# Performance work log

Measured on AMD Instinct MI355X. Metric: run time of the kernel, lower is better.

## Reference

```python
import jax, jax.numpy as jnp
import numpy as np

B, S, E, H = 2, 2048, 1024, 16
D = E // H

def setup_inputs() -> dict:
    key = jax.random.key(0)
    ks = jax.random.split(key, 5)
    return {
        "hidden_states": jax.random.normal(ks[0], (B, S, E), dtype=jnp.float32),
        "c_attn_w": jax.random.normal(ks[1], (E, 3 * E), dtype=jnp.float32) * 0.02,
        "c_attn_b": jax.random.normal(ks[2], (3 * E,), dtype=jnp.float32) * 0.02,
        "c_proj_w": jax.random.normal(ks[3], (E, E), dtype=jnp.float32) * 0.02,
        "c_proj_b": jax.random.normal(ks[4], (E,), dtype=jnp.float32) * 0.02,
    }

def reference(hidden_states, c_attn_w, c_attn_b, c_proj_w, c_proj_b):
    x = hidden_states                      # [B, S, E]
    b, s, _ = x.shape
    w_q, w_k, w_v = jnp.split(c_attn_w, 3, axis=1)   # each [E, E]
    q_b, k_b, v_b = jnp.split(c_attn_b, 3, axis=0)   # each [E]

    # value projection
    v = x @ w_v + v_b                                        # [B,S,E]
    v = v.reshape(b, s, H, D).transpose(0, 2, 1, 3)          # [B,H,S,D]

    # fused query: ((x Wq + qb) Wk^T + kb)
    q = (x @ w_q + q_b) @ w_k.T + k_b                        # [B,S,E]
    qh = q.reshape(b, s, H, D).transpose(0, 2, 1, 3)         # [B,H,S,D]

    # key side is RAW hidden states split per head
    kh = x.reshape(b, s, H, D).transpose(0, 2, 1, 3)         # [B,H,S,D]

    scale = 1.0 / jnp.float32(D) ** 0.5
    scores = jnp.einsum("bhqd,bhkd->bhqk",
                        qh.astype(jnp.float32),
                        kh.astype(jnp.float32)) * scale       # [B,H,S,S] fp32

    causal = jnp.tril(jnp.ones((s, s), dtype=bool))
    mask_value = jnp.finfo(jnp.float32).min
    scores = jnp.where(causal[None, None], scores, mask_value)

    probs = jax.nn.softmax(scores, axis=-1).astype(v.dtype)  # [B,H,S,S]

    out = jnp.einsum("bhqk,bhkd->bhqd", probs, v)            # [B,H,S,D]
    out = out.transpose(0, 2, 1, 3).reshape(b, s, E)         # [B,S,E]
    out = out @ c_proj_w + c_proj_b
    return out
```

## Files before the change

### kernel.cpp

```cpp
#include <hip/hip_runtime.h>

typedef __attribute__((ext_vector_type(8))) __bf16 bf16x8;
typedef __attribute__((ext_vector_type(4))) __bf16 bf16x4;
typedef __attribute__((ext_vector_type(4))) float f32x4;

typedef __attribute__((address_space(1))) void as1_void;
typedef __attribute__((address_space(3))) void as3_void;

__device__ __forceinline__ void gl_lds16(const void* g, void* l) {
    __builtin_amdgcn_global_load_lds((const as1_void*)g, (as3_void*)l, 16, 0, 0);
}

__device__ __forceinline__ const bf16x8* swz(const __bf16* base, int row, int chunk) {
    return (const bf16x8*)((const char*)base + row * 128 + ((chunk ^ (row & 7)) * 16));
}

#define QSCALE (0.125f * 1.44269504f)

__global__ __launch_bounds__(256) void prep_kernel(
    const float* __restrict__ x, const float* __restrict__ caw,
    const float* __restrict__ cab, const float* __restrict__ cpw,
    __bf16* __restrict__ xb, __bf16* __restrict__ wvt,
    __bf16* __restrict__ wkn, __bf16* __restrict__ wqn,
    __bf16* __restrict__ wpt, float* __restrict__ bqv)
{
    __shared__ float tile[32 * 33];
    int bid = blockIdx.x;
    int tid = threadIdx.x;
    if (bid < 1024) {
        int nt = bid >> 5, kt = bid & 31;
        int tx = tid & 31, ty = tid >> 5;
        int n0 = nt * 32, k0 = kt * 32;
#pragma unroll
        for (int i = 0; i < 4; ++i)
            tile[(ty + i * 8) * 33 + tx] = caw[(long)(k0 + ty + i * 8) * 3072 + 2048 + n0 + tx];
        __syncthreads();
#pragma unroll
        for (int i = 0; i < 4; ++i)
            wvt[(long)(n0 + ty + i * 8) * 1024 + k0 + tx] = (__bf16)tile[tx * 33 + ty + i * 8];
    } else if (bid < 2048) {
        int v = bid - 1024;
        int nt = v >> 5, kt = v & 31;
        int tx = tid & 31, ty = tid >> 5;
        int n0 = nt * 32, k0 = kt * 32;
#pragma unroll
        for (int i = 0; i < 4; ++i)
            tile[(ty + i * 8) * 33 + tx] = cpw[(long)(k0 + ty + i * 8) * 1024 + n0 + tx];
        __syncthreads();
#pragma unroll
        for (int i = 0; i < 4; ++i)
            wpt[(long)(n0 + ty + i * 8) * 1024 + k0 + tx] = (__bf16)tile[tx * 33 + ty + i * 8];
    } else if (bid < 3072) {
        int e = (bid - 2048) * 1024 + tid * 4;
        int n = e >> 10, k = e & 1023;
        float4 f = *(const float4*)(caw + (long)n * 3072 + 1024 + k);
        bf16x4 o = {(__bf16)f.x, (__bf16)f.y, (__bf16)f.z, (__bf16)f.w};
        *(bf16x4*)(wkn + e) = o;
    } else if (bid < 4096) {
        int e = (bid - 3072) * 1024 + tid * 4;
        int n = e >> 10, k = e & 1023;
        float4 f = *(const float4*)(caw + (long)n * 3072 + k);
        bf16x4 o = {(__bf16)f.x, (__bf16)f.y, (__bf16)f.z, (__bf16)f.w};
        *(bf16x4*)(wqn + e) = o;
    } else if (bid < 8192) {
        long e = (long)(bid - 4096) * 1024 + tid * 4;
        float4 f = *(const float4*)(x + e);
        bf16x4 o = {(__bf16)f.x, (__bf16)f.y, (__bf16)f.z, (__bf16)f.w};
        *(bf16x4*)(xb + e) = o;
    } else {
        int k = bid - 8192;
        int wave = tid >> 6, lane = tid & 63;
        float qv[16];
#pragma unroll
        for (int u = 0; u < 4; ++u) {
            float4 q4 = *(const float4*)(cab + u * 256 + lane * 4);
            qv[u * 4 + 0] = q4.x; qv[u * 4 + 1] = q4.y;
            qv[u * 4 + 2] = q4.z; qv[u * 4 + 3] = q4.w;
        }
        for (int i = 0; i < 16; ++i) {
            int n = k * 64 + wave * 16 + i;
            float s = 0.f;
#pragma unroll
            for (int u = 0; u < 4; ++u) {
                float4 w4 = *(const float4*)(caw + (long)n * 3072 + 1024 + u * 256 + lane * 4);
                s += w4.x * qv[u * 4 + 0] + w4.y * qv[u * 4 + 1]
                   + w4.z * qv[u * 4 + 2] + w4.w * qv[u * 4 + 3];
            }
#pragma unroll
            for (int off = 1; off < 64; off <<= 1) s += __shfl_xor(s, off);
            if (lane == 0) bqv[n] = (s + cab[1024 + n]) * QSCALE;
        }
        if (tid < 64) bqv[1024 + k * 64 + tid] = cab[2048 + k * 64 + tid];
    }
}

template <bool BF16OUT, int BN>
__global__ __launch_bounds__(256) void gemm_bt(
    const __bf16* __restrict__ A, int lda,
    const __bf16* __restrict__ B, int ldb,
    const float* __restrict__ bias,
    void* __restrict__ C, int ldc, int K, float oscale)
{
    constexpr int NT = BN / 32;
    __shared__ __bf16 As[128 * 64];
    __shared__ __bf16 Bs[BN * 64];
    const int tid = threadIdx.x;
    const int lane = tid & 63;
    const int wave = tid >> 6;
    const int quad = lane >> 4, l16 = lane & 15;
    const long m0 = (long)blockIdx.y * 128;
    const long n0 = (long)blockIdx.x * BN;
    const int wm = (wave >> 1) * 64, wn = (wave & 1) * (BN / 2);

    f32x4 acc[4][NT] = {};

    for (int k0 = 0; k0 < K; k0 += 64) {
#pragma unroll
        for (int c = tid; c < (128 + BN) * 8; c += 256) {
            int row = c >> 3, cc = (c & 7) ^ (row & 7);
            if (row < 128)
                gl_lds16(A + (m0 + row) * lda + k0 + cc * 8, As + c * 8);
            else
                gl_lds16(B + (n0 + row - 128) * ldb + k0 + cc * 8, Bs + (c - 1024) * 8);
        }
        __syncthreads();
#pragma unroll
        for (int kk = 0; kk < 2; ++kk) {
            bf16x8 af[4], bfr[NT];
#pragma unroll
            for (int i = 0; i < 4; ++i)
                af[i] = *swz(As, wm + i * 16 + l16, kk * 4 + quad);
#pragma unroll
            for (int j = 0; j < NT; ++j)
                bfr[j] = *swz(Bs, wn + j * 16 + l16, kk * 4 + quad);
#pragma unroll
            for (int i = 0; i < 4; ++i)
#pragma unroll
                for (int j = 0; j < NT; ++j)
                    acc[i][j] = __builtin_amdgcn_mfma_f32_16x16x32_bf16(af[i], bfr[j], acc[i][j], 0, 0, 0);
        }
        __syncthreads();
    }
#pragma unroll
    for (int i = 0; i < 4; ++i) {
        long row = m0 + wm + i * 16 + quad * 4;
#pragma unroll
        for (int j = 0; j < NT; ++j) {
            int col = (int)n0 + wn + j * 16 + l16;
            float bb = bias ? bias[col] : 0.f;
#pragma unroll
            for (int r = 0; r < 4; ++r) {
                float v = (acc[i][j][r] + bb) * oscale;
                if (BF16OUT)
                    ((__bf16*)C)[(row + r) * ldc + col] = (__bf16)v;
                else
                    ((float*)C)[(row + r) * ldc + col] = v;
            }
        }
    }
}

__global__ __launch_bounds__(256) void gemm_qv(
    const __bf16* __restrict__ A,
    const __bf16* __restrict__ B,
    const float* __restrict__ bias,
    __bf16* __restrict__ Qout,
    __bf16* __restrict__ VTout)
{
    __shared__ __bf16 smem[128 * 136];
    __bf16* As = smem;
    __bf16* Bs = smem + 8192;
    const int tid = threadIdx.x;
    const int lane = tid & 63;
    const int wave = tid >> 6;
    const int quad = lane >> 4, l16 = lane & 15;
    const long m0 = (long)blockIdx.y * 128;
    const long n0 = (long)blockIdx.x * 128;
    const int wm = (wave >> 1) * 64, wn = (wave & 1) * 64;

    f32x4 acc[4][4] = {};

    for (int k0 = 0; k0 < 1024; k0 += 64) {
#pragma unroll
        for (int c = tid; c < 2048; c += 256) {
            int row = c >> 3, cc = (c & 7) ^ (row & 7);
            if (row < 128)
                gl_lds16(A + (m0 + row) * 1024 + k0 + cc * 8, As + c * 8);
            else
                gl_lds16(B + (n0 + row - 128) * 1024 + k0 + cc * 8, Bs + (c - 1024) * 8);
        }
        __syncthreads();
#pragma unroll
        for (int kk = 0; kk < 2; ++kk) {
            bf16x8 af[4], bfr[4];
#pragma unroll
            for (int i = 0; i < 4; ++i)
                af[i] = *swz(As, wm + i * 16 + l16, kk * 4 + quad);
#pragma unroll
            for (int j = 0; j < 4; ++j)
                bfr[j] = *swz(Bs, wn + j * 16 + l16, kk * 4 + quad);
#pragma unroll
            for (int i = 0; i < 4; ++i)
#pragma unroll
                for (int j = 0; j < 4; ++j)
                    acc[i][j] = __builtin_amdgcn_mfma_f32_16x16x32_bf16(af[i], bfr[j], acc[i][j], 0, 0, 0);
        }
        __syncthreads();
    }

    if (n0 < 1024) {
#pragma unroll
        for (int i = 0; i < 4; ++i) {
            long row = m0 + wm + i * 16 + quad * 4;
#pragma unroll
            for (int j = 0; j < 4; ++j) {
                int col = (int)n0 + wn + j * 16 + l16;
                float bb = bias[col];
#pragma unroll
                for (int r = 0; r < 4; ++r)
                    Qout[(row + r) * 1024 + col] = (__bf16)(acc[i][j][r] + bb);
            }
        }
    } else {
        __syncthreads();
#pragma unroll
        for (int i = 0; i < 4; ++i) {
#pragma unroll
            for (int j = 0; j < 4; ++j) {
                int col = (int)n0 + wn + j * 16 + l16;
                float bb = bias[col];
                bf16x4 v;
#pragma unroll
                for (int r = 0; r < 4; ++r) v[r] = (__bf16)(acc[i][j][r] + bb);
                *(bf16x4*)(smem + (wn + j * 16 + l16) * 136 + wm + i * 16 + quad * 4) = v;
            }
        }
        __syncthreads();
        const int d0 = (int)n0 - 1024;
        const int bb = (int)(m0 >> 11);
        const int sl = (int)(m0 & 2047);
#pragma unroll
        for (int pass = 0; pass < 16; ++pass) {
            int idx = pass * 256 + tid;
            int n = idx >> 5;
            int mc = (idx & 31) * 4;
            bf16x4 v = *(const bf16x4*)(smem + n * 136 + mc);
            *(bf16x4*)(VTout + ((long)(bb * 1024 + d0 + n)) * 2048 + sl + mc) = v;
        }
    }
}

__global__ __launch_bounds__(512) void attn_kernel(
    const __bf16* __restrict__ Q,
    const __bf16* __restrict__ Xb,
    const __bf16* __restrict__ VT,
    __bf16* __restrict__ O)
{
    __shared__ __bf16 Ks[2 * 8192];
    __shared__ __bf16 Vs[2 * 8192];
    __shared__ __bf16 Ps[8 * 1024];
    const int tid = threadIdx.x;
    const int lane = tid & 63;
    const int wave = tid >> 6;
    const int group = wave >> 2;
    const int w4 = wave & 3;
    const int quad = lane >> 4, l16 = lane & 15;
    const int qa = blockIdx.y;
    const int qb = 31 - qa;
    const int qt = group ? qb : qa;
    const int bh = blockIdx.x;
    const int b = bh >> 4, h = bh & 15;
    const long rowbase = (long)b * 2048;

    const int s0 = tid;
    const int c0 = ((s0 & 7) ^ ((s0 >> 3) & 7)) * 8;

    bf16x8 ones;
#pragma unroll
    for (int i = 0; i < 8; ++i) ones[i] = (__bf16)1.0f;

    bf16x8 qfr[2];
    {
        const __bf16* qp = Q + (rowbase + qt * 64 + w4 * 16 + l16) * 1024 + h * 64 + quad * 8;
        qfr[0] = *(const bf16x8*)(qp);
        qfr[1] = *(const bf16x8*)(qp + 32);
    }

    const __bf16* kp0 = Xb + (rowbase + (s0 >> 3)) * 1024 + h * 64 + c0;
    const __bf16* vp0 = VT + ((long)(b * 1024 + h * 64 + (s0 >> 3))) * 2048 + c0;

    auto stage_tile = [&](int j, int buf, int sub) {
        gl_lds16(kp0 + (long)j * 65536, Ks + buf * 8192 + sub * 4096 + s0 * 8);
        gl_lds16(vp0 + j * 64, Vs + buf * 8192 + sub * 4096 + s0 * 8);
    };
    stage_tile(0, 0, 0);
    stage_tile(1, 0, 1);

    const int nouter = (qb + 2) >> 1;

    f32x4 oacc[4] = {};
    f32x4 lacc = {};
    __bf16* Pw = Ps + wave * 1024;

    for (int jj = 0; jj < nouter; ++jj) {
        __syncthreads();
        if (jj + 1 < nouter) {
            stage_tile(2 * jj + 2, (jj + 1) & 1, 0);
            stage_tile(2 * jj + 3, (jj + 1) & 1, 1);
        }

#pragma unroll
        for (int sub = 0; sub < 2; ++sub) {
            const int j = 2 * jj + sub;
            if (j > qt) continue;
            const __bf16* Kb = Ks + (jj & 1) * 8192 + sub * 4096;
            const __bf16* Vb = Vs + (jj & 1) * 8192 + sub * 4096;

            bf16x8 kf[2][4], vf[2][4];
#pragma unroll
            for (int kk = 0; kk < 2; ++kk)
#pragma unroll
                for (int kt = 0; kt < 4; ++kt) {
                    kf[kk][kt] = *swz(Kb, kt * 16 + l16, kk * 4 + quad);
                    vf[kk][kt] = *swz(Vb, kt * 16 + l16, kk * 4 + quad);
                }

            f32x4 sacc[4] = {};
            __builtin_amdgcn_s_setprio(1);
#pragma unroll
            for (int kk = 0; kk < 2; ++kk)
#pragma unroll
                for (int kt = 0; kt < 4; ++kt)
                    sacc[kt] = __builtin_amdgcn_mfma_f32_16x16x32_bf16(
                        kf[kk][kt], qfr[kk], sacc[kt], 0, 0, 0);
            __builtin_amdgcn_s_setprio(0);

            if (j == qt) {
                const int qloc = w4 * 16 + l16;
#pragma unroll
                for (int kt = 0; kt < 4; ++kt) {
                    bf16x4 pk;
#pragma unroll
                    for (int r = 0; r < 4; ++r) {
                        float s = sacc[kt][r];
                        if (kt * 16 + quad * 4 + r > qloc) s = -1e30f;
                        pk[r] = (__bf16)exp2f(s);
                    }
                    *(bf16x4*)((char*)Pw + l16 * 128 +
                               (((kt * 2 + (quad >> 1)) ^ (l16 & 7)) * 16) + (quad & 1) * 8) = pk;
                }
            } else {
#pragma unroll
                for (int kt = 0; kt < 4; ++kt) {
                    bf16x4 pk;
#pragma unroll
                    for (int r = 0; r < 4; ++r)
                        pk[r] = (__bf16)exp2f(sacc[kt][r]);
                    *(bf16x4*)((char*)Pw + l16 * 128 +
                               (((kt * 2 + (quad >> 1)) ^ (l16 & 7)) * 16) + (quad & 1) * 8) = pk;
                }
            }

            __builtin_amdgcn_s_setprio(1);
#pragma unroll
            for (int kk = 0; kk < 2; ++kk) {
                bf16x8 pf = *swz(Pw, l16, kk * 4 + quad);
                lacc = __builtin_amdgcn_mfma_f32_16x16x32_bf16(ones, pf, lacc, 0, 0, 0);
#pragma unroll
                for (int dt = 0; dt < 4; ++dt)
                    oacc[dt] = __builtin_amdgcn_mfma_f32_16x16x32_bf16(
                        vf[kk][dt], pf, oacc[dt], 0, 0, 0);
            }
            __builtin_amdgcn_s_setprio(0);
        }
    }

    {
        float inv = 1.0f / lacc[0];
        long row = rowbase + qt * 64 + w4 * 16 + l16;
#pragma unroll
        for (int dt = 0; dt < 4; ++dt) {
            bf16x4 ov;
#pragma unroll
            for (int r = 0; r < 4; ++r) ov[r] = (__bf16)(oacc[dt][r] * inv);
            *(bf16x4*)(O + row * 1024 + h * 64 + dt * 16 + quad * 4) = ov;
        }
    }
}

extern "C" void kernel_launch(void* const* d_in, const int* in_sizes, int n_in,
                              void* d_out, int out_size, void* d_ws, size_t ws_size,
                              hipStream_t stream) {
    const float* x   = (const float*)d_in[0];
    const float* caw = (const float*)d_in[1];
    const float* cab = (const float*)d_in[2];
    const float* cpw = (const float*)d_in[3];
    const float* cpb = (const float*)d_in[4];

    char* p = (char*)d_ws;
    auto alloc = [&](size_t bytes) {
        void* r = (void*)p;
        p += (bytes + 255) & ~(size_t)255;
        return r;
    };
    __bf16* xb    = (__bf16*)alloc(4096UL * 1024 * 2);
    __bf16* mtb   = (__bf16*)alloc(1024UL * 1024 * 2);
    __bf16* wvt   = (__bf16*)alloc(1024UL * 1024 * 2);
    __bf16* wkn   = (__bf16*)alloc(1024UL * 1024 * 2);
    __bf16* wqn   = (__bf16*)alloc(1024UL * 1024 * 2);
    __bf16* wpt   = (__bf16*)alloc(1024UL * 1024 * 2);
    float*  bqv   = (float*) alloc(2048UL * 4);
    __bf16* qbuf  = (__bf16*)alloc(4096UL * 1024 * 2);
    __bf16* vt    = (__bf16*)alloc(2048UL * 2048 * 2);
    __bf16* attn  = (__bf16*)alloc(4096UL * 1024 * 2);

    prep_kernel<<<8208, 256, 0, stream>>>(x, caw, cab, cpw, xb, wvt, wkn, wqn, wpt, bqv);

    gemm_bt<true, 32><<<dim3(32, 8), 256, 0, stream>>>(wkn, 1024, wqn, 1024, nullptr,
                                                       (void*)mtb, 1024, 1024, QSCALE);
    gemm_qv<<<dim3(16, 32), 256, 0, stream>>>(xb, mtb, bqv, qbuf, vt);
    attn_kernel<<<dim3(32, 16), 512, 0, stream>>>(qbuf, xb, vt, attn);
    gemm_bt<false, 64><<<dim3(16, 32), 256, 0, stream>>>(attn, 1024, wpt, 1024, cpb,
                                                         d_out, 1024, 1024, 1.0f);
    (void)in_sizes; (void)n_in; (void)out_size; (void)ws_size;
}
```

Baseline: 184.1 us.

## Fuse Wk·Wqᵀ weight GEMM into prep kernel with on-the-fly fp32→bf16 conversion

Removes the separate bf16 conversion of the Wq and Wk slices and the standalone gemm_bt launch that built the fused query matrix. Prep blocks now read fp32 weights directly, convert them to bf16 into LDS, and run the MFMA product inside the prep kernel. This saves one launch and the intermediate bf16 weight round-trip through memory. In exchange the new GEMM blocks use unpipelined synchronous loads, a larger shared-memory footprint for every prep block, and strided fp32 reads.

```diff
diff --git a/kernel.cpp b/kernel.cpp
--- a/kernel.cpp
+++ b/kernel.cpp
@@ -13,6 +13,14 @@
 
 __device__ __forceinline__ const bf16x8* swz(const __bf16* base, int row, int chunk) {
     return (const bf16x8*)((const char*)base + row * 128 + ((chunk ^ (row & 7)) * 16));
+}
+
+__device__ __forceinline__ bf16x8 cvt8(const float* p) {
+    float4 a = *(const float4*)p, b = *(const float4*)(p + 4);
+    bf16x8 o;
+    o[0] = (__bf16)a.x; o[1] = (__bf16)a.y; o[2] = (__bf16)a.z; o[3] = (__bf16)a.w;
+    o[4] = (__bf16)b.x; o[5] = (__bf16)b.y; o[6] = (__bf16)b.z; o[7] = (__bf16)b.w;
+    return o;
 }
 
 #define QSCALE (0.125f * 1.44269504f)
@@ -21,13 +29,14 @@
     const float* __restrict__ x, const float* __restrict__ caw,
     const float* __restrict__ cab, const float* __restrict__ cpw,
     __bf16* __restrict__ xb, __bf16* __restrict__ wvt,
-    __bf16* __restrict__ wkn, __bf16* __restrict__ wqn,
-    __bf16* __restrict__ wpt, float* __restrict__ bqv)
+    __bf16* __restrict__ wpt, float* __restrict__ bqv,
+    __bf16* __restrict__ mtb)
 {
-    __shared__ float tile[32 * 33];
+    __shared__ char smem_u[20480];
     int bid = blockIdx.x;
     int tid = threadIdx.x;
     if (bid < 1024) {
+        float* tile = (float*)smem_u;
         int nt = bid >> 5, kt = bid & 31;
         int tx = tid & 31, ty = tid >> 5;
         int n0 = nt * 32, k0 = kt * 32;
@@ -39,6 +48,7 @@
         for (int i = 0; i < 4; ++i)
             wvt[(long)(n0 + ty + i * 8) * 1024 + k0 + tx] = (__bf16)tile[tx * 33 + ty + i * 8];
     } else if (bid < 2048) {
+        float* tile = (float*)smem_u;
         int v = bid - 1024;
         int nt = v >> 5, kt = v & 31;
         int tx = tid & 31, ty = tid >> 5;
@@ -50,25 +60,13 @@
 #pragma unroll
         for (int i = 0; i < 4; ++i)
             wpt[(long)(n0 + ty + i * 8) * 1024 + k0 + tx] = (__bf16)tile[tx * 33 + ty + i * 8];
-    } else if (bid < 3072) {
-        int e = (bid - 2048) * 1024 + tid * 4;
-        int n = e >> 10, k = e & 1023;
-        float4 f = *(const float4*)(caw + (long)n * 3072 + 1024 + k);
-        bf16x4 o = {(__bf16)f.x, (__bf16)f.y, (__bf16)f.z, (__bf16)f.w};
-        *(bf16x4*)(wkn + e) = o;
-    } else if (bid < 4096) {
-        int e = (bid - 3072) * 1024 + tid * 4;
-        int n = e >> 10, k = e & 1023;
-        float4 f = *(const float4*)(caw + (long)n * 3072 + k);
-        bf16x4 o = {(__bf16)f.x, (__bf16)f.y, (__bf16)f.z, (__bf16)f.w};
-        *(bf16x4*)(wqn + e) = o;
-    } else if (bid < 8192) {
-        long e = (long)(bid - 4096) * 1024 + tid * 4;
+    } else if (bid < 6144) {
+        long e = (long)(bid - 2048) * 1024 + tid * 4;
         float4 f = *(const float4*)(x + e);
         bf16x4 o = {(__bf16)f.x, (__bf16)f.y, (__bf16)f.z, (__bf16)f.w};
         *(bf16x4*)(xb + e) = o;
-    } else {
-        int k = bid - 8192;
+    } else if (bid < 6160) {
+        int k = bid - 6144;
         int wave = tid >> 6, lane = tid & 63;
         float qv[16];
 #pragma unroll
@@ -91,6 +89,61 @@
             if (lane == 0) bqv[n] = (s + cab[1024 + n]) * QSCALE;
         }
         if (tid < 64) bqv[1024 + k * 64 + tid] = cab[2048 + k * 64 + tid];
+    } else {
+        __bf16* As = (__bf16*)smem_u;
+        __bf16* Bs = (__bf16*)(smem_u + 16384);
+        const int v = bid - 6160;
+        const int bx = v & 31, by = v >> 5;
+        const int lane = tid & 63;
+        const int wave = tid >> 6;
+        const int quad = lane >> 4, l16 = lane & 15;
+        const long m0 = (long)by * 128;
+        const long n0 = (long)bx * 32;
+        const int wm = (wave >> 1) * 64, wn = (wave & 1) * 16;
+
+        f32x4 acc[4] = {};
+
+        for (int k0 = 0; k0 < 1024; k0 += 64) {
+            bf16x8 st[5];
+#pragma unroll
+            for (int i = 0; i < 5; ++i) {
+                int c = tid + i * 256;
+                int row = c >> 3, cc = (c & 7) ^ (row & 7);
+                const float* src = (row < 128)
+                    ? caw + (long)(m0 + row) * 3072 + 1024 + k0 + cc * 8
+                    : caw + (long)(n0 + row - 128) * 3072 + k0 + cc * 8;
+                st[i] = cvt8(src);
+            }
+            __syncthreads();
+#pragma unroll
+            for (int i = 0; i < 5; ++i) {
+                int c = tid + i * 256;
+                int row = c >> 3;
+                if (row < 128) *(bf16x8*)(As + c * 8) = st[i];
+                else           *(bf16x8*)(Bs + (c - 1024) * 8) = st[i];
+            }
+            __syncthreads();
+#pragma unroll
+            for (int kk = 0; kk < 2; ++kk) {
+                bf16x8 af[4], bfr;
+#pragma unroll
+                for (int i = 0; i < 4; ++i)
+                    af[i] = *swz(As, wm + i * 16 + l16, kk * 4 + quad);
+                bfr = *swz(Bs, wn + l16, kk * 4 + quad);
+#pragma unroll
+                for (int i = 0; i < 4; ++i)
+                    acc[i] = __builtin_amdgcn_mfma_f32_16x16x32_bf16(af[i], bfr, acc[i], 0, 0, 0);
+            }
+            __syncthreads();
+        }
+#pragma unroll
+        for (int i = 0; i < 4; ++i) {
+            long row = m0 + wm + i * 16 + quad * 4;
+            int col = (int)n0 + wn + l16;
+#pragma unroll
+            for (int r = 0; r < 4; ++r)
+                mtb[(row + r) * 1024 + col] = (__bf16)(acc[i][r] * QSCALE);
+        }
     }
 }
 
@@ -406,18 +459,13 @@
     __bf16* xb    = (__bf16*)alloc(4096UL * 1024 * 2);
     __bf16* mtb   = (__bf16*)alloc(1024UL * 1024 * 2);
     __bf16* wvt   = (__bf16*)alloc(1024UL * 1024 * 2);
-    __bf16* wkn   = (__bf16*)alloc(1024UL * 1024 * 2);
-    __bf16* wqn   = (__bf16*)alloc(1024UL * 1024 * 2);
     __bf16* wpt   = (__bf16*)alloc(1024UL * 1024 * 2);
     float*  bqv   = (float*) alloc(2048UL * 4);
     __bf16* qbuf  = (__bf16*)alloc(4096UL * 1024 * 2);
     __bf16* vt    = (__bf16*)alloc(2048UL * 2048 * 2);
     __bf16* attn  = (__bf16*)alloc(4096UL * 1024 * 2);
 
-    prep_kernel<<<8208, 256, 0, stream>>>(x, caw, cab, cpw, xb, wvt, wkn, wqn, wpt, bqv);
-
-    gemm_bt<true, 32><<<dim3(32, 8), 256, 0, stream>>>(wkn, 1024, wqn, 1024, nullptr,
-                                                       (void*)mtb, 1024, 1024, QSCALE);
+    prep_kernel<<<6416, 256, 0, stream>>>(x, caw, cab, cpw, xb, wvt, wpt, bqv, mtb);
     gemm_qv<<<dim3(16, 32), 256, 0, stream>>>(xb, mtb, bqv, qbuf, vt);
     attn_kernel<<<dim3(32, 16), 512, 0, stream>>>(qbuf, xb, vt, attn);
     gemm_bt<false, 64><<<dim3(16, 32), 256, 0, stream>>>(attn, 1024, wpt, 1024, cpb,
```

Result: slower. 189.1 us (+2.8%).

## Compute query as (xWq+qb)Wk^T+kb instead of precomposing WqWk^T

Applied to the files above, without the earlier changes.

Drops the precomputed fused matrix Wq·Wk^T and the bias GEMV blocks in the prep kernel. It instead runs a full x·Wq+qb GEMM into a temporary buffer, then multiplies that by Wk^T (plus kb and the softmax scale) inside the Q/V GEMM, which now takes a separate A operand per half. This removes the small weight-product GEMM and the per-row bias reduction. In exchange it adds a full-size activation GEMM and an extra round-trip of a 4096x1024 intermediate through memory.

```diff
diff --git a/kernel.cpp b/kernel.cpp
--- a/kernel.cpp
+++ b/kernel.cpp
@@ -19,10 +19,10 @@
 
 __global__ __launch_bounds__(256) void prep_kernel(
     const float* __restrict__ x, const float* __restrict__ caw,
-    const float* __restrict__ cab, const float* __restrict__ cpw,
+    const float* __restrict__ cpw,
     __bf16* __restrict__ xb, __bf16* __restrict__ wvt,
-    __bf16* __restrict__ wkn, __bf16* __restrict__ wqn,
-    __bf16* __restrict__ wpt, float* __restrict__ bqv)
+    __bf16* __restrict__ wpt, __bf16* __restrict__ wqt,
+    __bf16* __restrict__ wkn)
 {
     __shared__ float tile[32 * 33];
     int bid = blockIdx.x;
@@ -51,46 +51,28 @@
         for (int i = 0; i < 4; ++i)
             wpt[(long)(n0 + ty + i * 8) * 1024 + k0 + tx] = (__bf16)tile[tx * 33 + ty + i * 8];
     } else if (bid < 3072) {
-        int e = (bid - 2048) * 1024 + tid * 4;
+        int v = bid - 2048;
+        int nt = v >> 5, kt = v & 31;
+        int tx = tid & 31, ty = tid >> 5;
+        int n0 = nt * 32, k0 = kt * 32;
+#pragma unroll
+        for (int i = 0; i < 4; ++i)
+            tile[(ty + i * 8) * 33 + tx] = caw[(long)(k0 + ty + i * 8) * 3072 + n0 + tx];
+        __syncthreads();
+#pragma unroll
+        for (int i = 0; i < 4; ++i)
+            wqt[(long)(n0 + ty + i * 8) * 1024 + k0 + tx] = (__bf16)tile[tx * 33 + ty + i * 8];
+    } else if (bid < 4096) {
+        int e = (bid - 3072) * 1024 + tid * 4;
         int n = e >> 10, k = e & 1023;
         float4 f = *(const float4*)(caw + (long)n * 3072 + 1024 + k);
         bf16x4 o = {(__bf16)f.x, (__bf16)f.y, (__bf16)f.z, (__bf16)f.w};
         *(bf16x4*)(wkn + e) = o;
-    } else if (bid < 4096) {
-        int e = (bid - 3072) * 1024 + tid * 4;
-        int n = e >> 10, k = e & 1023;
-        float4 f = *(const float4*)(caw + (long)n * 3072 + k);
-        bf16x4 o = {(__bf16)f.x, (__bf16)f.y, (__bf16)f.z, (__bf16)f.w};
-        *(bf16x4*)(wqn + e) = o;
-    } else if (bid < 8192) {
+    } else {
         long e = (long)(bid - 4096) * 1024 + tid * 4;
         float4 f = *(const float4*)(x + e);
         bf16x4 o = {(__bf16)f.x, (__bf16)f.y, (__bf16)f.z, (__bf16)f.w};
         *(bf16x4*)(xb + e) = o;
-    } else {
-        int k = bid - 8192;
-        int wave = tid >> 6, lane = tid & 63;
-        float qv[16];
-#pragma unroll
-        for (int u = 0; u < 4; ++u) {
-            float4 q4 = *(const float4*)(cab + u * 256 + lane * 4);
-            qv[u * 4 + 0] = q4.x; qv[u * 4 + 1] = q4.y;
-            qv[u * 4 + 2] = q4.z; qv[u * 4 + 3] = q4.w;
-        }
-        for (int i = 0; i < 16; ++i) {
-            int n = k * 64 + wave * 16 + i;
-            float s = 0.f;
-#pragma unroll
-            for (int u = 0; u < 4; ++u) {
-                float4 w4 = *(const float4*)(caw + (long)n * 3072 + 1024 + u * 256 + lane * 4);
-                s += w4.x * qv[u * 4 + 0] + w4.y * qv[u * 4 + 1]
-                   + w4.z * qv[u * 4 + 2] + w4.w * qv[u * 4 + 3];
-            }
-#pragma unroll
-            for (int off = 1; off < 64; off <<= 1) s += __shfl_xor(s, off);
-            if (lane == 0) bqv[n] = (s + cab[1024 + n]) * QSCALE;
-        }
-        if (tid < 64) bqv[1024 + k * 64 + tid] = cab[2048 + k * 64 + tid];
     }
 }
 
@@ -161,7 +143,8 @@
 }
 
 __global__ __launch_bounds__(256) void gemm_qv(
-    const __bf16* __restrict__ A,
+    const __bf16* __restrict__ Aq,
+    const __bf16* __restrict__ Av,
     const __bf16* __restrict__ B,
     const float* __restrict__ bias,
     __bf16* __restrict__ Qout,
@@ -177,6 +160,8 @@
     const long m0 = (long)blockIdx.y * 128;
     const long n0 = (long)blockIdx.x * 128;
     const int wm = (wave >> 1) * 64, wn = (wave & 1) * 64;
+    const __bf16* A = (n0 < 1024) ? Aq : Av;
+    const float osc = (n0 < 1024) ? QSCALE : 1.0f;
 
     f32x4 acc[4][4] = {};
 
@@ -218,7 +203,7 @@
                 float bb = bias[col];
 #pragma unroll
                 for (int r = 0; r < 4; ++r)
-                    Qout[(row + r) * 1024 + col] = (__bf16)(acc[i][j][r] + bb);
+                    Qout[(row + r) * 1024 + col] = (__bf16)((acc[i][j][r] + bb) * osc);
             }
         }
     } else {
@@ -404,23 +389,20 @@
         return r;
     };
     __bf16* xb    = (__bf16*)alloc(4096UL * 1024 * 2);
-    __bf16* mtb   = (__bf16*)alloc(1024UL * 1024 * 2);
+    __bf16* wkn   = (__bf16*)alloc(1024UL * 1024 * 2);
     __bf16* wvt   = (__bf16*)alloc(1024UL * 1024 * 2);
-    __bf16* wkn   = (__bf16*)alloc(1024UL * 1024 * 2);
-    __bf16* wqn   = (__bf16*)alloc(1024UL * 1024 * 2);
+    __bf16* wqt   = (__bf16*)alloc(1024UL * 1024 * 2);
     __bf16* wpt   = (__bf16*)alloc(1024UL * 1024 * 2);
-    float*  bqv   = (float*) alloc(2048UL * 4);
+    __bf16* tb    = (__bf16*)alloc(4096UL * 1024 * 2);
     __bf16* qbuf  = (__bf16*)alloc(4096UL * 1024 * 2);
     __bf16* vt    = (__bf16*)alloc(2048UL * 2048 * 2);
-    __bf16* attn  = (__bf16*)alloc(4096UL * 1024 * 2);
-
-    prep_kernel<<<8208, 256, 0, stream>>>(x, caw, cab, cpw, xb, wvt, wkn, wqn, wpt, bqv);
-
-    gemm_bt<true, 32><<<dim3(32, 8), 256, 0, stream>>>(wkn, 1024, wqn, 1024, nullptr,
-                                                       (void*)mtb, 1024, 1024, QSCALE);
-    gemm_qv<<<dim3(16, 32), 256, 0, stream>>>(xb, mtb, bqv, qbuf, vt);
-    attn_kernel<<<dim3(32, 16), 512, 0, stream>>>(qbuf, xb, vt, attn);
-    gemm_bt<false, 64><<<dim3(16, 32), 256, 0, stream>>>(attn, 1024, wpt, 1024, cpb,
+
+    prep_kernel<<<8192, 256, 0, stream>>>(x, caw, cpw, xb, wvt, wpt, wqt, wkn);
+    gemm_bt<true, 64><<<dim3(16, 32), 256, 0, stream>>>(xb, 1024, wqt, 1024, cab,
+                                                        (void*)tb, 1024, 1024, 1.0f);
+    gemm_qv<<<dim3(16, 32), 256, 0, stream>>>(tb, xb, wkn, cab + 1024, qbuf, vt);
+    attn_kernel<<<dim3(32, 16), 512, 0, stream>>>(qbuf, xb, vt, tb);
+    gemm_bt<false, 64><<<dim3(16, 32), 256, 0, stream>>>(tb, 1024, wpt, 1024, cpb,
                                                          d_out, 1024, 1024, 1.0f);
     (void)in_sizes; (void)n_in; (void)out_size; (void)ws_size;
 }
```

Result: no change. 181.2 us (-1.5%).
